# Kernel tuning notes

Hardware: AMD Instinct MI355X
Metric: run time of the kernel (lower is better)

The kernel has to match this reference:

```python
import jax, jax.numpy as jnp
import numpy as np

# so(3) generators (3x3x3), L[s, r, a]
L = jnp.array([[[0, 0, 0], [0, 0, -1], [0, 1, 0]],
               [[0, 0, 1], [0, 0, 0], [-1, 0, 0]],
               [[0, -1, 0], [1, 0, 0], [0, 0, 0]]], dtype=jnp.float32)


def setup_inputs() -> dict:
    key = jax.random.key(0)
    B, S, X, Y = 32, 3, 512, 512
    s = jax.random.normal(key, (B, S, X, Y), dtype=jnp.float32)
    # normalize to unit O(3) spins (physically realistic; math identical for any s)
    s = s / jnp.linalg.norm(s, axis=1, keepdims=True)
    t = jnp.ones((1,), dtype=jnp.float32)   # flow time
    c0 = jnp.ones((1,), dtype=jnp.float32)  # learnable coefficient C[0]
    return {"s": s, "t": t, "c0": c0}


def reference(s, t, c0):
    # Psi11t.grad(s, t): flow force of the (psi_1^1)^2 action term.
    # Coeff(t) with EvenOdd=False and cc=[c0] is t * c0.
    coeff = t * c0  # shape [1], broadcasts

    def nbr(x, mu):
        # sum of forward and backward periodic neighbors along lattice axis mu
        return jnp.roll(x, -1, axis=mu) + jnp.roll(x, 1, axis=mu)

    # b[b,x,y] = sum_mu s . (s shifted +/- along mu)
    b = (jnp.einsum('bsxy,bsxy->bxy', s, nbr(s, 2))
         + jnp.einsum('bsxy,bsxy->bxy', s, nbr(s, 3)))

    bs = s * b[:, None]  # [B,3,X,Y]

    # Lsig[b,r,a,x,y] = -sum_s s[b,s,x,y] * L[s,r,a]
    Lsig = -jnp.einsum('bsxy,sra->braxy', s, L)

    Fs = nbr(s, 2) + nbr(s, 3)      # [B,3,X,Y]
    Fbs = nbr(bs, 2) + nbr(bs, 3)   # [B,3,X,Y]

    F = Fs * b[:, None] + Fbs
    F = jnp.einsum('bsaxy,bsxy->baxy', Lsig, F)  # so(3) generator contraction
    return 2.0 * coeff * F
```

## Files before the change

kernel.cpp:

```cpp
#include <hip/hip_runtime.h>

#define BATCH 32
#define NX 512
#define NY 512
#define XY (NX * NY)
#define TX 8
#define ROWS (TX + 4)

__global__ __launch_bounds__(256) void psi11t_kernel(
    const float* __restrict__ s,
    const float* __restrict__ t,
    const float* __restrict__ c0,
    float* __restrict__ out)
{
    __shared__ float lds[3][ROWS][NY];

    const int tid   = threadIdx.x;
    const int strip = blockIdx.x;
    const int bidx  = blockIdx.y;
    const int x0    = strip * TX;
    const float* sb = s + (size_t)bidx * 3 * XY;

    for (int f = tid; f < 3 * ROWS * (NY / 4); f += 256) {
        int c   = f / (ROWS * (NY / 4));
        int rem = f - c * (ROWS * (NY / 4));
        int r   = rem / (NY / 4);
        int v   = rem - r * (NY / 4);
        int gx  = x0 + r - 2;
        if (gx < 0)   gx += NX;
        if (gx >= NX) gx -= NX;
        float4 val = *(const float4*)(sb + (size_t)c * XY + (size_t)gx * NY + 4 * v);
        *(float4*)(&lds[c][r][4 * v]) = val;
    }
    __syncthreads();

    const float coeff = 2.0f * t[0] * c0[0];
    const int ty = tid & 127;
    const int rx = tid >> 7;
    const int y0 = ty * 4;

    for (int it = 0; it < TX / 2; ++it) {
        int lr = 2 + it * 2 + rx;
        int gx = x0 + it * 2 + rx;

        float wc[3][8], am[3][6], ap[3][6], a2m[3][4], a2p[3][4];
        #pragma unroll
        for (int c = 0; c < 3; ++c) {
            #pragma unroll
            for (int j = 0; j < 8; ++j)
                wc[c][j] = lds[c][lr][(y0 - 2 + j) & (NY - 1)];
            #pragma unroll
            for (int j = 0; j < 6; ++j) {
                am[c][j] = lds[c][lr - 1][(y0 - 1 + j) & (NY - 1)];
                ap[c][j] = lds[c][lr + 1][(y0 - 1 + j) & (NY - 1)];
            }
            #pragma unroll
            for (int j = 0; j < 4; ++j) {
                a2m[c][j] = lds[c][lr - 2][(y0 + j) & (NY - 1)];
                a2p[c][j] = lds[c][lr + 2][(y0 + j) & (NY - 1)];
            }
        }

        float o[3][4];
        #pragma unroll
        for (int i = 0; i < 4; ++i) {
            float sc[3], sA[3], sB[3], sC[3], sD[3], Fs[3];
            float bc = 0.f, bA = 0.f, bB = 0.f, bC = 0.f, bD = 0.f;
            #pragma unroll
            for (int c = 0; c < 3; ++c) {
                sc[c] = wc[c][2 + i];
                sA[c] = am[c][1 + i];
                sB[c] = ap[c][1 + i];
                sC[c] = wc[c][1 + i];
                sD[c] = wc[c][3 + i];
                float sAA = a2m[c][i];
                float sBB = a2p[c][i];
                float sCC = wc[c][i];
                float sDD = wc[c][4 + i];
                float sAC = am[c][i];
                float sAD = am[c][2 + i];
                float sBC = ap[c][i];
                float sBD = ap[c][2 + i];
                float nsum = sA[c] + sB[c] + sC[c] + sD[c];
                Fs[c] = nsum;
                bc += sc[c] * nsum;
                bA += sA[c] * (sAA + sc[c] + sAC + sAD);
                bB += sB[c] * (sc[c] + sBB + sBC + sBD);
                bC += sC[c] * (sAC + sBC + sCC + sc[c]);
                bD += sD[c] * (sAD + sBD + sc[c] + sDD);
            }
            float G[3];
            #pragma unroll
            for (int c = 0; c < 3; ++c)
                G[c] = Fs[c] * bc + sA[c] * bA + sB[c] * bB + sC[c] * bC + sD[c] * bD;
            o[0][i] = (sc[1] * G[2] - sc[2] * G[1]) * coeff;
            o[1][i] = (sc[2] * G[0] - sc[0] * G[2]) * coeff;
            o[2][i] = (sc[0] * G[1] - sc[1] * G[0]) * coeff;
        }

        float* ob = out + (size_t)bidx * 3 * XY + (size_t)gx * NY + y0;
        *(float4*)(ob)          = make_float4(o[0][0], o[0][1], o[0][2], o[0][3]);
        *(float4*)(ob + XY)     = make_float4(o[1][0], o[1][1], o[1][2], o[1][3]);
        *(float4*)(ob + 2 * XY) = make_float4(o[2][0], o[2][1], o[2][2], o[2][3]);
    }
}

extern "C" void kernel_launch(void* const* d_in, const int* in_sizes, int n_in,
                              void* d_out, int out_size, void* d_ws, size_t ws_size,
                              hipStream_t stream) {
    const float* s  = (const float*)d_in[0];
    const float* t  = (const float*)d_in[1];
    const float* c0 = (const float*)d_in[2];
    float* out = (float*)d_out;

    dim3 grid(NX / TX, BATCH);
    psi11t_kernel<<<grid, 256, 0, stream>>>(s, t, c0, out);
}
```

Before: 208.5 us.

## Replace LDS-tiled stencil with direct global float4 loads per thread

```diff
diff --git a/kernel.cpp b/kernel.cpp
--- a/kernel.cpp
+++ b/kernel.cpp
@@ -4,8 +4,6 @@
 #define NX 512
 #define NY 512
 #define XY (NX * NY)
-#define TX 8
-#define ROWS (TX + 4)
 
 __global__ __launch_bounds__(256) void psi11t_kernel(
     const float* __restrict__ s,
@@ -13,96 +11,90 @@
     const float* __restrict__ c0,
     float* __restrict__ out)
 {
-    __shared__ float lds[3][ROWS][NY];
+    const int tid  = threadIdx.x;
+    const int yg   = tid & 127;
+    const int xr   = tid >> 7;
+    const int y0   = yg * 4;
+    const int x    = blockIdx.x * 2 + xr;
+    const int bidx = blockIdx.y;
 
-    const int tid   = threadIdx.x;
-    const int strip = blockIdx.x;
-    const int bidx  = blockIdx.y;
-    const int x0    = strip * TX;
+    const int xm1 = (x + NX - 1) & (NX - 1);
+    const int xp1 = (x + 1)      & (NX - 1);
+    const int xm2 = (x + NX - 2) & (NX - 1);
+    const int xp2 = (x + 2)      & (NX - 1);
+    const int om4 = (y0 + NY - 4) & (NY - 1);
+    const int op4 = (y0 + 4)      & (NY - 1);
+
     const float* sb = s + (size_t)bidx * 3 * XY;
 
-    for (int f = tid; f < 3 * ROWS * (NY / 4); f += 256) {
-        int c   = f / (ROWS * (NY / 4));
-        int rem = f - c * (ROWS * (NY / 4));
-        int r   = rem / (NY / 4);
-        int v   = rem - r * (NY / 4);
-        int gx  = x0 + r - 2;
-        if (gx < 0)   gx += NX;
-        if (gx >= NX) gx -= NX;
-        float4 val = *(const float4*)(sb + (size_t)c * XY + (size_t)gx * NY + 4 * v);
-        *(float4*)(&lds[c][r][4 * v]) = val;
+    float cm[3][12], um[3][12], dm[3][12], u2[3][4], d2[3][4];
+
+    #pragma unroll
+    for (int c = 0; c < 3; ++c) {
+        const float* base = sb + (size_t)c * XY;
+        const float* rc  = base + (size_t)x   * NY;
+        const float* rm  = base + (size_t)xm1 * NY;
+        const float* rp  = base + (size_t)xp1 * NY;
+        const float* rm2 = base + (size_t)xm2 * NY;
+        const float* rp2 = base + (size_t)xp2 * NY;
+
+        *(float4*)&cm[c][0] = *(const float4*)(rc + om4);
+        *(float4*)&cm[c][4] = *(const float4*)(rc + y0);
+        *(float4*)&cm[c][8] = *(const float4*)(rc + op4);
+        *(float4*)&um[c][0] = *(const float4*)(rm + om4);
+        *(float4*)&um[c][4] = *(const float4*)(rm + y0);
+        *(float4*)&um[c][8] = *(const float4*)(rm + op4);
+        *(float4*)&dm[c][0] = *(const float4*)(rp + om4);
+        *(float4*)&dm[c][4] = *(const float4*)(rp + y0);
+        *(float4*)&dm[c][8] = *(const float4*)(rp + op4);
+        *(float4*)&u2[c][0] = *(const float4*)(rm2 + y0);
+        *(float4*)&d2[c][0] = *(const float4*)(rp2 + y0);
     }
-    __syncthreads();
 
     const float coeff = 2.0f * t[0] * c0[0];
-    const int ty = tid & 127;
-    const int rx = tid >> 7;
-    const int y0 = ty * 4;
 
-    for (int it = 0; it < TX / 2; ++it) {
-        int lr = 2 + it * 2 + rx;
-        int gx = x0 + it * 2 + rx;
-
-        float wc[3][8], am[3][6], ap[3][6], a2m[3][4], a2p[3][4];
+    float o[3][4];
+    #pragma unroll
+    for (int i = 0; i < 4; ++i) {
+        float sc[3], sA[3], sB[3], sC[3], sD[3], Fs[3];
+        float bc = 0.f, bA = 0.f, bB = 0.f, bC = 0.f, bD = 0.f;
         #pragma unroll
         for (int c = 0; c < 3; ++c) {
-            #pragma unroll
-            for (int j = 0; j < 8; ++j)
-                wc[c][j] = lds[c][lr][(y0 - 2 + j) & (NY - 1)];
-            #pragma unroll
-            for (int j = 0; j < 6; ++j) {
-                am[c][j] = lds[c][lr - 1][(y0 - 1 + j) & (NY - 1)];
-                ap[c][j] = lds[c][lr + 1][(y0 - 1 + j) & (NY - 1)];
-            }
-            #pragma unroll
-            for (int j = 0; j < 4; ++j) {
-                a2m[c][j] = lds[c][lr - 2][(y0 + j) & (NY - 1)];
-                a2p[c][j] = lds[c][lr + 2][(y0 + j) & (NY - 1)];
-            }
+            sc[c] = cm[c][4 + i];
+            sC[c] = cm[c][3 + i];
+            sD[c] = cm[c][5 + i];
+            float sCC = cm[c][2 + i];
+            float sDD = cm[c][6 + i];
+            sA[c] = um[c][4 + i];
+            float sAC = um[c][3 + i];
+            float sAD = um[c][5 + i];
+            sB[c] = dm[c][4 + i];
+            float sBC = dm[c][3 + i];
+            float sBD = dm[c][5 + i];
+            float sAA = u2[c][i];
+            float sBB = d2[c][i];
+
+            float nsum = sA[c] + sB[c] + sC[c] + sD[c];
+            Fs[c] = nsum;
+            bc += sc[c] * nsum;
+            bA += sA[c] * (sAA + sc[c] + sAC + sAD);
+            bB += sB[c] * (sc[c] + sBB + sBC + sBD);
+            bC += sC[c] * (sAC + sBC + sCC + sc[c]);
+            bD += sD[c] * (sAD + sBD + sc[c] + sDD);
         }
+        float G[3];
+        #pragma unroll
+        for (int c = 0; c < 3; ++c)
+            G[c] = Fs[c] * bc + sA[c] * bA + sB[c] * bB + sC[c] * bC + sD[c] * bD;
+        o[0][i] = (sc[1] * G[2] - sc[2] * G[1]) * coeff;
+        o[1][i] = (sc[2] * G[0] - sc[0] * G[2]) * coeff;
+        o[2][i] = (sc[0] * G[1] - sc[1] * G[0]) * coeff;
+    }
 
-        float o[3][4];
-        #pragma unroll
-        for (int i = 0; i < 4; ++i) {
-            float sc[3], sA[3], sB[3], sC[3], sD[3], Fs[3];
-            float bc = 0.f, bA = 0.f, bB = 0.f, bC = 0.f, bD = 0.f;
-            #pragma unroll
-            for (int c = 0; c < 3; ++c) {
-                sc[c] = wc[c][2 + i];
-                sA[c] = am[c][1 + i];
-                sB[c] = ap[c][1 + i];
-                sC[c] = wc[c][1 + i];
-                sD[c] = wc[c][3 + i];
-                float sAA = a2m[c][i];
-                float sBB = a2p[c][i];
-                float sCC = wc[c][i];
-                float sDD = wc[c][4 + i];
-                float sAC = am[c][i];
-                float sAD = am[c][2 + i];
-                float sBC = ap[c][i];
-                float sBD = ap[c][2 + i];
-                float nsum = sA[c] + sB[c] + sC[c] + sD[c];
-                Fs[c] = nsum;
-                bc += sc[c] * nsum;
-                bA += sA[c] * (sAA + sc[c] + sAC + sAD);
-                bB += sB[c] * (sc[c] + sBB + sBC + sBD);
-                bC += sC[c] * (sAC + sBC + sCC + sc[c]);
-                bD += sD[c] * (sAD + sBD + sc[c] + sDD);
-            }
-            float G[3];
-            #pragma unroll
-            for (int c = 0; c < 3; ++c)
-                G[c] = Fs[c] * bc + sA[c] * bA + sB[c] * bB + sC[c] * bC + sD[c] * bD;
-            o[0][i] = (sc[1] * G[2] - sc[2] * G[1]) * coeff;
-            o[1][i] = (sc[2] * G[0] - sc[0] * G[2]) * coeff;
-            o[2][i] = (sc[0] * G[1] - sc[1] * G[0]) * coeff;
-        }
-
-        float* ob = out + (size_t)bidx * 3 * XY + (size_t)gx * NY + y0;
-        *(float4*)(ob)          = make_float4(o[0][0], o[0][1], o[0][2], o[0][3]);
-        *(float4*)(ob + XY)     = make_float4(o[1][0], o[1][1], o[1][2], o[1][3]);
-        *(float4*)(ob + 2 * XY) = make_float4(o[2][0], o[2][1], o[2][2], o[2][3]);
-    }
+    float* ob = out + (size_t)bidx * 3 * XY + (size_t)x * NY + y0;
+    *(float4*)(ob)          = make_float4(o[0][0], o[0][1], o[0][2], o[0][3]);
+    *(float4*)(ob + XY)     = make_float4(o[1][0], o[1][1], o[1][2], o[1][3]);
+    *(float4*)(ob + 2 * XY) = make_float4(o[2][0], o[2][1], o[2][2], o[2][3]);
 }
 
 extern "C" void kernel_launch(void* const* d_in, const int* in_sizes, int n_in,
@@ -113,6 +105,6 @@
     const float* c0 = (const float*)d_in[2];
     float* out = (float*)d_out;
 
-    dim3 grid(NX / TX, BATCH);
+    dim3 grid(NX / 2, BATCH);
     psi11t_kernel<<<grid, 256, 0, stream>>>(s, t, c0, out);
 }
```

After: 209.9 us. No clear change (+0.7%).
